# Kernel tuning notes

Hardware: AMD Instinct MI355X
Metric: run time of the kernel (lower is better)

## Reference

```python
import jax, jax.numpy as jnp
import numpy as np

B, T_ENC, T_DEC = 32, 128, 32
V_SRC, V_TGT = 32000, 32000
E_SRC, E_TGT = 256, 256
H_ENC, H_DEC, A = 512, 512, 8
CTX = 2 * H_ENC  # bidirectional encoder output dim


def setup_inputs():
    key = jax.random.key(0)
    ks = jax.random.split(key, 24)
    s = jnp.float32(0.02)

    def rn(k, shape):
        return jax.random.normal(k, shape, jnp.float32) * s

    return {
        'encoder_inputs': jax.random.randint(ks[0], (B, T_ENC), 0, V_SRC),
        'encoder_seq_length': jax.random.randint(ks[1], (B,), 1, T_ENC + 1),
        'decoder_inputs': jax.random.randint(ks[2], (B, T_DEC), 0, V_TGT),
        'decoder_seq_length': jax.random.randint(ks[3], (B,), 1, T_DEC + 1),
        'emb_src': rn(ks[4], (V_SRC, E_SRC)).at[0].set(0.0),  # padding_idx=0
        'emb_tgt': rn(ks[5], (V_TGT, E_TGT)).at[0].set(0.0),
        'Wih_f': rn(ks[6], (4 * H_ENC, E_SRC)), 'Whh_f': rn(ks[7], (4 * H_ENC, H_ENC)),
        'bih_f': rn(ks[8], (4 * H_ENC,)), 'bhh_f': rn(ks[9], (4 * H_ENC,)),
        'Wih_b': rn(ks[10], (4 * H_ENC, E_SRC)), 'Whh_b': rn(ks[11], (4 * H_ENC, H_ENC)),
        'bih_b': rn(ks[12], (4 * H_ENC,)), 'bhh_b': rn(ks[13], (4 * H_ENC,)),
        'gru_Wih': rn(ks[14], (3 * H_DEC, E_TGT + CTX)), 'gru_Whh': rn(ks[15], (3 * H_DEC, H_DEC)),
        'gru_bih': rn(ks[16], (3 * H_DEC,)), 'gru_bhh': rn(ks[17], (3 * H_DEC,)),
        'attn_W': rn(ks[18], (CTX + H_DEC, A)), 'attn_b': rn(ks[19], (A,)),
        'attn_v': rn(ks[20], (A,)),
        'clf_W': rn(ks[21], (V_TGT, H_DEC)), 'clf_b': rn(ks[22], (V_TGT,)),
    }


def _lstm(x_tbe, Wih, Whh, bih, bhh):
    # x_tbe: [T, B, E] -> hidden outputs [T, B, H]; PyTorch gate order i,f,g,o
    Bz = x_tbe.shape[1]
    h0 = jnp.zeros((Bz, H_ENC), x_tbe.dtype)

    def step(carry, xt):
        h, c = carry
        g = xt @ Wih.T + bih + h @ Whh.T + bhh
        i, f, gg, o = jnp.split(g, 4, axis=-1)
        c = jax.nn.sigmoid(f) * c + jax.nn.sigmoid(i) * jnp.tanh(gg)
        h = jax.nn.sigmoid(o) * jnp.tanh(c)
        return (h, c), h

    _, hs = jax.lax.scan(step, (h0, h0), x_tbe)
    return hs


def _gru(x, h, Wih, Whh, bih, bhh):
    # PyTorch GRUCell: gates r, z, n
    gi = x @ Wih.T + bih
    gh = h @ Whh.T + bhh
    ir, iz, inn = jnp.split(gi, 3, axis=-1)
    hr, hz, hn = jnp.split(gh, 3, axis=-1)
    r = jax.nn.sigmoid(ir + hr)
    z = jax.nn.sigmoid(iz + hz)
    n = jnp.tanh(inn + r * hn)
    return (1.0 - z) * n + z * h


def reference(encoder_inputs, encoder_seq_length, decoder_inputs, decoder_seq_length,
              emb_src, emb_tgt,
              Wih_f, Whh_f, bih_f, bhh_f, Wih_b, Whh_b, bih_b, bhh_b,
              gru_Wih, gru_Whh, gru_bih, gru_bhh,
              attn_W, attn_b, attn_v, clf_W, clf_b):
    lens = encoder_seq_length
    x = emb_src[encoder_inputs]                                   # [B,T,E]
    t = jnp.arange(T_ENC)[None, :]
    valid = t < lens[:, None]                                     # [B,T]

    # forward LSTM (padded steps masked out below; they never affect valid outputs)
    h_f = jnp.swapaxes(_lstm(jnp.swapaxes(x, 0, 1), Wih_f, Whh_f, bih_f, bhh_f), 0, 1)
    # backward LSTM: reverse each sequence within its true length
    rev = jnp.where(valid, lens[:, None] - 1 - t, t)              # [B,T]
    x_r = jnp.take_along_axis(x, rev[:, :, None], axis=1)
    h_b = jnp.swapaxes(_lstm(jnp.swapaxes(x_r, 0, 1), Wih_b, Whh_b, bih_b, bhh_b), 0, 1)
    h_b = jnp.take_along_axis(h_b, rev[:, :, None], axis=1)
    # pad_packed_sequence zeroes outputs past seq length
    enc_out = jnp.concatenate([h_f, h_b], axis=-1) * valid[:, :, None].astype(x.dtype)  # [B,T,2H]

    NEG = jnp.float32(-1e9)

    def step(h, tok):
        # ConcatAttention: v^T tanh(W [enc_out; state] + b), masked softmax
        feat = jnp.concatenate(
            [enc_out, jnp.broadcast_to(h[:, None, :], (B, T_ENC, H_DEC))], axis=-1)
        e = jnp.tanh(feat @ attn_W + attn_b) @ attn_v             # [B,T]
        a = jax.nn.softmax(jnp.where(valid, e, NEG), axis=-1)
        ctx = jnp.einsum('bt,btd->bd', a, enc_out)                # [B,2H]
        # pre-concat decoder: GRUCell([emb; ctx], h)
        xin = jnp.concatenate([emb_tgt[tok], ctx], axis=-1)
        h_new = _gru(xin, h, gru_Wih, gru_Whh, gru_bih, gru_bhh)
        logit = jax.nn.relu(h_new @ clf_W.T + clf_b)              # [B,V]
        return h_new, logit

    h0 = jnp.zeros((B, H_DEC), jnp.float32)
    _, outs = jax.lax.scan(step, h0, jnp.swapaxes(decoder_inputs, 0, 1))
    return jnp.swapaxes(outs, 0, 1)                               # [B,T_dec,V_tgt]
```

## Files before the change

kernel.cpp:

```cpp
#include <hip/hip_runtime.h>
#include <cmath>

#define NB   32
#define TE   128
#define TD   32
#define VOC  32000
#define EMB  256
#define HH   512
#define CTXD 1024
#define NR   1536

#define OHS  2048
#define OEO  (OHS + 2*129*NB*HH)
#define OEP  (OEO + NB*TE*CTXD)
#define OHD  (OEP + NB*TE*8)
#define OVEO (OHD + (TD+1)*NB*HH)
#define WSEND (OVEO + NB*NR*TE/2)

__device__ __forceinline__ float sigf(float x) { return 1.0f / (1.0f + expf(-x)); }
__device__ __forceinline__ float hsum4(float4 v) { return (v.x + v.y) + (v.z + v.w); }

__device__ __forceinline__ void stg1(float* p, float v) {
  __hip_atomic_store(p, v, __ATOMIC_RELAXED, __HIP_MEMORY_SCOPE_AGENT);
}

__device__ __forceinline__ void fma4(float4& a, const float4 w, const float4 u) {
  a.x = fmaf(w.x, u.x, a.x); a.y = fmaf(w.y, u.y, a.y);
  a.z = fmaf(w.z, u.z, a.z); a.w = fmaf(w.w, u.w, a.w);
}

__device__ __forceinline__ unsigned short to_bf16(float f) {
  unsigned int u = __float_as_uint(f);
  u = (u + 0x7FFF + ((u >> 16) & 1)) >> 16;
  return (unsigned short)u;
}

__device__ __forceinline__ void gbarG(int* bar, int idx, int target) {
  __syncthreads();
  if (threadIdx.x == 0) {
    __hip_atomic_fetch_add(bar + (idx & 7) * 16, 1,
                           __ATOMIC_RELAXED, __HIP_MEMORY_SCOPE_AGENT);
  }
  if (threadIdx.x < 64) {
    const int ln = threadIdx.x;
    int it = 0;
    while (true) {
      int v = (ln < 8)
        ? __hip_atomic_load(bar + ln * 16, __ATOMIC_RELAXED, __HIP_MEMORY_SCOPE_AGENT)
        : 0;
      v += __shfl_xor(v, 1); v += __shfl_xor(v, 2); v += __shfl_xor(v, 4);
      v = __shfl(v, 0);
      if (v >= target) break;
      __builtin_amdgcn_s_sleep(1);
      if (++it > (1 << 20)) break;
    }
  }
  __syncthreads();
}

__global__ void __launch_bounds__(512)
scan_kernel(const int* __restrict__ enc_in, const int* __restrict__ lens,
            const float* __restrict__ emb_src,
            const float* __restrict__ Wih_f, const float* __restrict__ Whh_f,
            const float* __restrict__ bih_f, const float* __restrict__ bhh_f,
            const float* __restrict__ Wih_b, const float* __restrict__ Whh_b,
            const float* __restrict__ bih_b, const float* __restrict__ bhh_b,
            float* __restrict__ ws)
{
  const int tid = threadIdx.x, bid = blockIdx.x;
  const int g = bid & 7, cg = bid >> 3;
  const int dir = g >> 2, bg = g & 3;
  int* bar = (int*)ws + g * 128;
  float* harr = ws + OHS;
  float* eo   = ws + OEO;

  asm volatile("buffer_inv sc1" ::: "memory");

  __shared__ int   tokL[TE][8];
  __shared__ float lds_p[8][4][68];

  for (int i = tid; i < TE * 8; i += 512) {
    int bb = i & 7, s = i >> 3;
    int b = bg * 8 + bb;
    int t = s;
    if (dir) { int L = lens[b]; t = (s < L) ? (L - 1 - s) : s; }
    tokL[s][bb] = enc_in[b * TE + t];
  }
  if (tid < 128) {
    int bb = tid >> 4, col = tid & 15;
    stg1(&harr[((size_t)(dir * 129) * NB + bg * 8 + bb) * HH + cg * 16 + col], 0.0f);
  }

  const int lane = tid & 63, w = tid >> 6;
  const int ks = w & 3, rh = w >> 2;
  const int rq = lane >> 4, kl = lane & 15;
  const int j0 = cg * 16;
  const float* Wih = dir ? Wih_b : Wih_f;
  const float* Whh = dir ? Whh_b : Whh_f;

  float4 Wreg[8][3];
  #pragma unroll
  for (int ri = 0; ri < 8; ++ri) {
    int r = rh * 32 + rq * 8 + ri;
    int o = (r >> 4) * HH + j0 + (r & 15);
    #pragma unroll
    for (int p = 0; p < 3; ++p) {
      int kf = (ks * 3 + p) * 16 + kl;
      Wreg[ri][p] = (kf < 64)
        ? *((const float4*)Wih + (size_t)o * 64 + kf)
        : *((const float4*)Whh + (size_t)o * 128 + (kf - 64));
    }
  }

  const int b_u = tid >> 4, col_u = tid & 15;
  const int j_u = j0 + col_u;
  const int bglob = bg * 8 + b_u;
  const int Lu = (tid < 128) ? lens[bglob] : 0;
  float bs0 = 0, bs1 = 0, bs2 = 0, bs3 = 0;
  if (tid < 128) {
    const float* bih = dir ? bih_b : bih_f;
    const float* bhh = dir ? bhh_b : bhh_f;
    bs0 = bih[j_u] + bhh[j_u];
    bs1 = bih[HH + j_u] + bhh[HH + j_u];
    bs2 = bih[2 * HH + j_u] + bhh[2 * HH + j_u];
    bs3 = bih[3 * HH + j_u] + bhh[3 * HH + j_u];
  }
  float cst = 0.0f;

  int tgt = 32;
  gbarG(bar, cg, tgt); tgt += 32;

  for (int s = 0; s < TE; ++s) {
    const float4* h4 = (const float4*)(harr + ((size_t)(dir * 129 + s) * NB) * HH);
    #pragma unroll 2
    for (int bb = 0; bb < 8; ++bb) {
      const int b = bg * 8 + bb;
      const int tok = tokL[s][bb];
      const float4* x4 = (const float4*)emb_src + (size_t)tok * 64;
      float4 u[3];
      #pragma unroll
      for (int p = 0; p < 3; ++p) {
        int c = ks * 3 + p;
        u[p] = (c < 4) ? x4[c * 16 + kl]
                       : h4[(size_t)b * 128 + (c - 4) * 16 + kl];
      }
      float sc[8];
      #pragma unroll
      for (int ri = 0; ri < 8; ++ri) {
        float4 a = {0, 0, 0, 0};
        fma4(a, Wreg[ri][0], u[0]);
        fma4(a, Wreg[ri][1], u[1]);
        fma4(a, Wreg[ri][2], u[2]);
        sc[ri] = hsum4(a);
      }
      #pragma unroll
      for (int ri = 0; ri < 8; ++ri) {
        sc[ri] += __shfl_xor(sc[ri], 1);
        sc[ri] += __shfl_xor(sc[ri], 2);
        sc[ri] += __shfl_xor(sc[ri], 4);
        sc[ri] += __shfl_xor(sc[ri], 8);
      }
      if (kl == 0) {
        int r0 = rh * 32 + rq * 8;
        float4 lo = {sc[0], sc[1], sc[2], sc[3]};
        float4 hi = {sc[4], sc[5], sc[6], sc[7]};
        *(float4*)&lds_p[bb][ks][r0]     = lo;
        *(float4*)&lds_p[bb][ks][r0 + 4] = hi;
      }
    }
    __syncthreads();

    if (tid < 128) {
      float gi = bs0, gf = bs1, gg = bs2, go = bs3;
      #pragma unroll
      for (int k2 = 0; k2 < 4; ++k2) {
        gi += lds_p[b_u][k2][col_u];
        gf += lds_p[b_u][k2][16 + col_u];
        gg += lds_p[b_u][k2][32 + col_u];
        go += lds_p[b_u][k2][48 + col_u];
      }
      float c = sigf(gf) * cst + sigf(gi) * tanhf(gg);
      cst = c;
      float h = sigf(go) * tanhf(c);
      stg1(&harr[((size_t)(dir * 129 + s + 1) * NB + bglob) * HH + j_u], h);
      float hm = (s < Lu) ? h : 0.0f;
      int pos = dir ? ((s < Lu) ? (Lu - 1 - s) : s) : s;
      eo[((size_t)bglob * TE + pos) * CTXD + dir * HH + j_u] = hm;
    }
    gbarG(bar, cg, tgt); tgt += 32;
  }
}

__global__ void __launch_bounds__(256)
veo_kernel(const float* __restrict__ eo, const float* __restrict__ gWih,
           unsigned short* __restrict__ veo)
{
  asm volatile("buffer_inv sc1" ::: "memory");
  __shared__ __align__(16) float As[16][132];
  __shared__ __align__(16) float Bs[16][132];
  const int tid = threadIdx.x;
  const int tx = tid & 15, ty = tid >> 4;
  const int n0 = blockIdx.x * 128, m0 = blockIdx.y * 128;
  float acc[8][8] = {};
  const int lr = tid >> 1;
  const int lk = (tid & 1) * 8;
  const float* arow = eo + (size_t)(m0 + lr) * CTXD;
  const float* brow = gWih + (size_t)(n0 + lr) * (EMB + CTXD) + EMB;

  for (int kc = 0; kc < CTXD; kc += 16) {
    float4 av0 = *(const float4*)&arow[kc + lk];
    float4 av1 = *(const float4*)&arow[kc + lk + 4];
    float4 bv0 = *(const float4*)&brow[kc + lk];
    float4 bv1 = *(const float4*)&brow[kc + lk + 4];
    __syncthreads();
    As[lk + 0][lr] = av0.x; As[lk + 1][lr] = av0.y;
    As[lk + 2][lr] = av0.z; As[lk + 3][lr] = av0.w;
    As[lk + 4][lr] = av1.x; As[lk + 5][lr] = av1.y;
    As[lk + 6][lr] = av1.z; As[lk + 7][lr] = av1.w;
    Bs[lk + 0][lr] = bv0.x; Bs[lk + 1][lr] = bv0.y;
    Bs[lk + 2][lr] = bv0.z; Bs[lk + 3][lr] = bv0.w;
    Bs[lk + 4][lr] = bv1.x; Bs[lk + 5][lr] = bv1.y;
    Bs[lk + 6][lr] = bv1.z; Bs[lk + 7][lr] = bv1.w;
    __syncthreads();
    #pragma unroll
    for (int kk = 0; kk < 16; ++kk) {
      float a8[8], b8[8];
      *(float4*)&a8[0] = *(const float4*)&As[kk][ty * 8];
      *(float4*)&a8[4] = *(const float4*)&As[kk][ty * 8 + 4];
      *(float4*)&b8[0] = *(const float4*)&Bs[kk][tx * 8];
      *(float4*)&b8[4] = *(const float4*)&Bs[kk][tx * 8 + 4];
      #pragma unroll
      for (int i = 0; i < 8; ++i)
        #pragma unroll
        for (int j = 0; j < 8; ++j)
          acc[i][j] = fmaf(a8[i], b8[j], acc[i][j]);
    }
  }
  const int b = m0 >> 7;
  #pragma unroll
  for (int j = 0; j < 8; ++j) {
    int n = n0 + tx * 8 + j;
    unsigned short o8[8];
    #pragma unroll
    for (int i = 0; i < 8; ++i) o8[i] = to_bf16(acc[i][j]);
    *(uint4*)&veo[((size_t)b * NR + n) * TE + ty * 8] = *(uint4*)o8;
  }
}

__global__ void __launch_bounds__(512)
dec_kernel(const int* __restrict__ dec_in, const int* __restrict__ lens,
           const float* __restrict__ emb_tgt,
           const float* __restrict__ gWih, const float* __restrict__ gWhh,
           const float* __restrict__ gbih, const float* __restrict__ gbhh,
           const float* __restrict__ attn_W, const float* __restrict__ attn_b,
           const float* __restrict__ attn_v,
           float* __restrict__ ws)
{
  const int tid = threadIdx.x, bid = blockIdx.x;
  const int g = bid & 7, cg = bid >> 3;
  const int B4 = g * 4;
  int* bar = (int*)ws + 1024 + g * 128;
  float* eo = ws + OEO;
  float* ep = ws + OEP;
  float* hd = ws + OHD;
  const unsigned short* veoH = (const unsigned short*)(ws + OVEO);

  asm volatile("buffer_inv sc1" ::: "memory");

  __shared__ float hl[4][520];
  __shared__ int   tokD[TD][4];
  __shared__ int   lensh[4];
  __shared__ float av8v[8];
  __shared__ float hpv[4][8];
  __shared__ float elds[4][128];
  __shared__ float wlds[4][128];
  __shared__ float mxs[4], invs[4];
  __shared__ float gvc[4][48];
  __shared__ float lds_pd[2][4][4][52];

  for (int i = tid; i < TD * 4; i += 512)
    tokD[i >> 2][i & 3] = dec_in[(B4 + (i & 3)) * TD + (i >> 2)];
  if (tid < 8) av8v[tid] = attn_v[tid];
  if (tid < 4) lensh[tid] = lens[B4 + tid];

  if (tid < 64) {
    int bb = tid >> 4, col = tid & 15;
    stg1(&hd[(size_t)(B4 + bb) * HH + cg * 16 + col], 0.0f);
  }

  {
    const int idx = cg * 512 + tid;
    if (idx < 4 * TE * 8) {
      int a = idx & 7, t = (idx >> 3) & 127, bb = idx >> 10;
      int b = B4 + bb;
      float acc = attn_b[a];
      const float* er = &eo[((size_t)b * TE + t) * CTXD];
      for (int d = 0; d < CTXD; d += 4) {
        float4 ev = *(const float4*)&er[d];
        acc = fmaf(ev.x, attn_W[(d + 0) * 8 + a], acc);
        acc = fmaf(ev.y, attn_W[(d + 1) * 8 + a], acc);
        acc = fmaf(ev.z, attn_W[(d + 2) * 8 + a], acc);
        acc = fmaf(ev.w, attn_W[(d + 3) * 8 + a], acc);
      }
      stg1(&ep[((size_t)b * TE + t) * 8 + a], acc);
    }
  }

  const int lane = tid & 63, w = tid >> 6;
  const int ks = w & 3, rh = w >> 2;
  const int rq = lane >> 4, kl = lane & 15;
  float4 Wreg[6][3];
  #pragma unroll
  for (int ri = 0; ri < 6; ++ri) {
    int rr = rh * 24 + rq * 6 + ri;
    int row = (rr >> 4) * HH + cg * 16 + (rr & 15);
    #pragma unroll
    for (int p = 0; p < 3; ++p) {
      int c = ks * 3 + p;
      Wreg[ri][p] = (c < 4)
        ? *(const float4*)(gWih + (size_t)row * (EMB + CTXD) + c * 64 + kl * 4)
        : *(const float4*)(gWhh + (size_t)row * HH + (c - 4) * 64 + kl * 4);
    }
  }

  const int ub = tid >> 4, ucol = tid & 15;
  const int uj = cg * 16 + ucol;
  float bRc = 0, bZc = 0, bNi = 0, bNh = 0;
  if (tid < 64) {
    bRc = gbih[uj] + gbhh[uj];
    bZc = gbih[HH + uj] + gbhh[HH + uj];
    bNi = gbih[2 * HH + uj];
    bNh = gbhh[2 * HH + uj];
  }

  int tgt = 32;
  gbarG(bar, cg, tgt); tgt += 32;

  for (int s = 0; s < TD; ++s) {
    {
      int bb = tid >> 7, c4 = (tid & 127) * 4;
      *(float4*)&hl[bb][c4] =
        *(const float4*)&hd[((size_t)s * NB + B4 + bb) * HH + c4];
    }
    __syncthreads();
    {
      const int bb = w >> 1;
      const float4* h4 = (const float4*)&hl[bb][0];
      float4 ha = h4[lane * 2], hb = h4[lane * 2 + 1];
      #pragma unroll
      for (int i = 0; i < 4; ++i) {
        const int a = (w & 1) * 4 + i;
        const float* wa = attn_W + (size_t)(CTXD + lane * 8) * 8 + a;
        float acc = 0.0f;
        acc = fmaf(ha.x, wa[0],  acc); acc = fmaf(ha.y, wa[8],  acc);
        acc = fmaf(ha.z, wa[16], acc); acc = fmaf(ha.w, wa[24], acc);
        acc = fmaf(hb.x, wa[32], acc); acc = fmaf(hb.y, wa[40], acc);
        acc = fmaf(hb.z, wa[48], acc); acc = fmaf(hb.w, wa[56], acc);
        acc += __shfl_xor(acc, 1);  acc += __shfl_xor(acc, 2);
        acc += __shfl_xor(acc, 4);  acc += __shfl_xor(acc, 8);
        acc += __shfl_xor(acc, 16); acc += __shfl_xor(acc, 32);
        if (lane == 0) hpv[bb][a] = acc;
      }
    }
    __syncthreads();
    {
      const int bb = tid >> 7, t = tid & 127;
      const int b = B4 + bb;
      float evv = -1e9f;
      if (t < lensh[bb]) {
        const float* e8 = &ep[((size_t)b * TE + t) * 8];
        float4 ea = *(const float4*)e8, eb2 = *(const float4*)(e8 + 4);
        evv  = tanhf(ea.x + hpv[bb][0]) * av8v[0];
        evv += tanhf(ea.y + hpv[bb][1]) * av8v[1];
        evv += tanhf(ea.z + hpv[bb][2]) * av8v[2];
        evv += tanhf(ea.w + hpv[bb][3]) * av8v[3];
        evv += tanhf(eb2.x + hpv[bb][4]) * av8v[4];
        evv += tanhf(eb2.y + hpv[bb][5]) * av8v[5];
        evv += tanhf(eb2.z + hpv[bb][6]) * av8v[6];
        evv += tanhf(eb2.w + hpv[bb][7]) * av8v[7];
      }
      elds[bb][t] = evv;
    }
    __syncthreads();
    if (tid < 256) {
      const int bb = tid >> 6, i = tid & 63;
      float m = fmaxf(elds[bb][i], elds[bb][i + 64]);
      m = fmaxf(m, __shfl_xor(m, 1));  m = fmaxf(m, __shfl_xor(m, 2));
      m = fmaxf(m, __shfl_xor(m, 4));  m = fmaxf(m, __shfl_xor(m, 8));
      m = fmaxf(m, __shfl_xor(m, 16)); m = fmaxf(m, __shfl_xor(m, 32));
      if (i == 0) mxs[bb] = m;
    }
    __syncthreads();
    {
      const int bb = tid >> 7, t = tid & 127;
      wlds[bb][t] = expf(elds[bb][t] - mxs[bb]);
    }
    __syncthreads();
    if (tid < 256) {
      const int bb = tid >> 6, i = tid & 63;
      float sm = wlds[bb][i] + wlds[bb][i + 64];
      sm += __shfl_xor(sm, 1);  sm += __shfl_xor(sm, 2);
      sm += __shfl_xor(sm, 4);  sm += __shfl_xor(sm, 8);
      sm += __shfl_xor(sm, 16); sm += __shfl_xor(sm, 32);
      if (i == 0) invs[bb] = 1.0f / sm;
    }
    {
      #pragma unroll
      for (int bb = 0; bb < 4; ++bb) {
        const float4* xr = (const float4*)(emb_tgt + (size_t)tokD[s][bb] * EMB);
        float4 u[3];
        #pragma unroll
        for (int p = 0; p < 3; ++p) {
          int c = ks * 3 + p;
          u[p] = (c < 4) ? xr[c * 16 + kl]
                         : *(const float4*)&hl[bb][(c - 4) * 64 + kl * 4];
        }
        float sI[6], sH[6];
        #pragma unroll
        for (int ri = 0; ri < 6; ++ri) {
          float4 aI = {0,0,0,0}, aH = {0,0,0,0};
          #pragma unroll
          for (int p = 0; p < 3; ++p) {
            int c = ks * 3 + p;
            if (c < 4) fma4(aI, Wreg[ri][p], u[p]);
            else       fma4(aH, Wreg[ri][p], u[p]);
          }
          sI[ri] = hsum4(aI); sH[ri] = hsum4(aH);
        }
        #pragma unroll
        for (int ri = 0; ri < 6; ++ri) {
          sI[ri] += __shfl_xor(sI[ri], 1); sH[ri] += __shfl_xor(sH[ri], 1);
          sI[ri] += __shfl_xor(sI[ri], 2); sH[ri] += __shfl_xor(sH[ri], 2);
          sI[ri] += __shfl_xor(sI[ri], 4); sH[ri] += __shfl_xor(sH[ri], 4);
          sI[ri] += __shfl_xor(sI[ri], 8); sH[ri] += __shfl_xor(sH[ri], 8);
        }
        if (kl == 0) {
          int r0 = rh * 24 + rq * 6;
          #pragma unroll
          for (int ri = 0; ri < 6; ++ri) {
            lds_pd[0][bb][ks][r0 + ri] = sI[ri];
            lds_pd[1][bb][ks][r0 + ri] = sH[ri];
          }
        }
      }
    }
    __syncthreads();
    if (tid < 384) {
      const int bb = tid / 96, idx = tid % 96;
      const int rr = idx >> 1, th = idx & 1;
      const int n = (rr >> 4) * HH + cg * 16 + (rr & 15);
      const unsigned short* vp = veoH + ((size_t)(B4 + bb) * NR + n) * TE + th * 64;
      const float* wl = &wlds[bb][th * 64];
      float acc = 0.0f;
      #pragma unroll
      for (int q = 0; q < 8; ++q) {
        uint4 pk = *(const uint4*)&vp[q * 8];
        unsigned int uu[4] = {pk.x, pk.y, pk.z, pk.w};
        #pragma unroll
        for (int h2 = 0; h2 < 4; ++h2) {
          acc = fmaf(wl[q * 8 + h2 * 2 + 0],
                     __uint_as_float((uu[h2] & 0xFFFFu) << 16), acc);
          acc = fmaf(wl[q * 8 + h2 * 2 + 1],
                     __uint_as_float((uu[h2] >> 16) << 16), acc);
        }
      }
      acc += __shfl_xor(acc, 1);
      if (th == 0) gvc[bb][rr] = acc * invs[bb];
    }
    __syncthreads();
    if (tid < 64) {
      float giR = gvc[ub][ucol], ghR = 0;
      float giZ = gvc[ub][16 + ucol], ghZ = 0;
      float giN = gvc[ub][32 + ucol], ghN = 0;
      #pragma unroll
      for (int k2 = 0; k2 < 4; ++k2) {
        giR += lds_pd[0][ub][k2][ucol];      ghR += lds_pd[1][ub][k2][ucol];
        giZ += lds_pd[0][ub][k2][16 + ucol]; ghZ += lds_pd[1][ub][k2][16 + ucol];
        giN += lds_pd[0][ub][k2][32 + ucol]; ghN += lds_pd[1][ub][k2][32 + ucol];
      }
      float r = sigf(giR + ghR + bRc);
      float z = sigf(giZ + ghZ + bZc);
      float n = tanhf(giN + bNi + r * (ghN + bNh));
      float hnew = (1.0f - z) * n + z * hl[ub][uj];
      stg1(&hd[((size_t)(s + 1) * NB + B4 + ub) * HH + uj], hnew);
    }
    gbarG(bar, cg, tgt); tgt += 32;
  }
}

__global__ void __launch_bounds__(256)
clf_kernel(const float* __restrict__ hd, const float* __restrict__ W,
           const float* __restrict__ bias, float* __restrict__ out)
{
  asm volatile("buffer_inv sc1" ::: "memory");
  __shared__ __align__(16) float As[16][132];
  __shared__ __align__(16) float Bs[16][132];
  const int tid = threadIdx.x;
  const int tx = tid & 15, ty = tid >> 4;
  const int n0 = blockIdx.x * 128, m0 = blockIdx.y * 128;
  float acc[8][8] = {};
  const int lr = tid >> 1;
  const int lk = (tid & 1) * 8;
  const int r  = m0 + lr;
  const float* arow = hd + ((size_t)((r & 31) + 1) * NB + (r >> 5)) * HH;
  const float* brow = W + (size_t)(n0 + lr) * HH;

  for (int kc = 0; kc < HH; kc += 16) {
    float4 av0 = *(const float4*)&arow[kc + lk];
    float4 av1 = *(const float4*)&arow[kc + lk + 4];
    float4 bv0 = *(const float4*)&brow[kc + lk];
    float4 bv1 = *(const float4*)&brow[kc + lk + 4];
    __syncthreads();
    As[lk + 0][lr] = av0.x; As[lk + 1][lr] = av0.y;
    As[lk + 2][lr] = av0.z; As[lk + 3][lr] = av0.w;
    As[lk + 4][lr] = av1.x; As[lk + 5][lr] = av1.y;
    As[lk + 6][lr] = av1.z; As[lk + 7][lr] = av1.w;
    Bs[lk + 0][lr] = bv0.x; Bs[lk + 1][lr] = bv0.y;
    Bs[lk + 2][lr] = bv0.z; Bs[lk + 3][lr] = bv0.w;
    Bs[lk + 4][lr] = bv1.x; Bs[lk + 5][lr] = bv1.y;
    Bs[lk + 6][lr] = bv1.z; Bs[lk + 7][lr] = bv1.w;
    __syncthreads();
    #pragma unroll
    for (int kk = 0; kk < 16; ++kk) {
      float a8[8], b8[8];
      *(float4*)&a8[0] = *(const float4*)&As[kk][ty * 8];
      *(float4*)&a8[4] = *(const float4*)&As[kk][ty * 8 + 4];
      *(float4*)&b8[0] = *(const float4*)&Bs[kk][tx * 8];
      *(float4*)&b8[4] = *(const float4*)&Bs[kk][tx * 8 + 4];
      #pragma unroll
      for (int i = 0; i < 8; ++i)
        #pragma unroll
        for (int j = 0; j < 8; ++j)
          acc[i][j] = fmaf(a8[i], b8[j], acc[i][j]);
    }
  }
  const int col = n0 + tx * 8;
  float bb[8];
  *(float4*)&bb[0] = *(const float4*)&bias[col];
  *(float4*)&bb[4] = *(const float4*)&bias[col + 4];
  #pragma unroll
  for (int i = 0; i < 8; ++i) {
    int row = m0 + ty * 8 + i;
    float4 o0, o1;
    o0.x = fmaxf(acc[i][0] + bb[0], 0.0f); o0.y = fmaxf(acc[i][1] + bb[1], 0.0f);
    o0.z = fmaxf(acc[i][2] + bb[2], 0.0f); o0.w = fmaxf(acc[i][3] + bb[3], 0.0f);
    o1.x = fmaxf(acc[i][4] + bb[4], 0.0f); o1.y = fmaxf(acc[i][5] + bb[5], 0.0f);
    o1.z = fmaxf(acc[i][6] + bb[6], 0.0f); o1.w = fmaxf(acc[i][7] + bb[7], 0.0f);
    *(float4*)&out[(size_t)row * VOC + col]     = o0;
    *(float4*)&out[(size_t)row * VOC + col + 4] = o1;
  }
}

extern "C" void kernel_launch(void* const* d_in, const int* in_sizes, int n_in,
                              void* d_out, int out_size, void* d_ws, size_t ws_size,
                              hipStream_t stream)
{
  if (ws_size < (size_t)WSEND * 4) return;

  const int* enc_in  = (const int*)d_in[0];
  const int* enc_len = (const int*)d_in[1];
  const int* dec_in  = (const int*)d_in[2];
  const float* emb_src = (const float*)d_in[4];
  const float* emb_tgt = (const float*)d_in[5];
  const float* Wih_f = (const float*)d_in[6];
  const float* Whh_f = (const float*)d_in[7];
  const float* bih_f = (const float*)d_in[8];
  const float* bhh_f = (const float*)d_in[9];
  const float* Wih_b = (const float*)d_in[10];
  const float* Whh_b = (const float*)d_in[11];
  const float* bih_b = (const float*)d_in[12];
  const float* bhh_b = (const float*)d_in[13];
  const float* gWih  = (const float*)d_in[14];
  const float* gWhh  = (const float*)d_in[15];
  const float* gbih  = (const float*)d_in[16];
  const float* gbhh  = (const float*)d_in[17];
  const float* attn_W = (const float*)d_in[18];
  const float* attn_b = (const float*)d_in[19];
  const float* attn_v = (const float*)d_in[20];
  const float* clf_W = (const float*)d_in[21];
  const float* clf_b = (const float*)d_in[22];
  float* ws  = (float*)d_ws;
  float* out = (float*)d_out;

  hipMemsetAsync(d_ws, 0, 8192, stream);
  scan_kernel<<<256, 512, 0, stream>>>(enc_in, enc_len, emb_src,
      Wih_f, Whh_f, bih_f, bhh_f, Wih_b, Whh_b, bih_b, bhh_b, ws);
  veo_kernel<<<dim3(NR / 128, (NB * TE) / 128), 256, 0, stream>>>(
      ws + OEO, gWih, (unsigned short*)(ws + OVEO));
  dec_kernel<<<256, 512, 0, stream>>>(dec_in, enc_len, emb_tgt,
      gWih, gWhh, gbih, gbhh, attn_W, attn_b, attn_v, ws);
  dim3 cg(VOC / 128, (NB * TD) / 128);
  clf_kernel<<<cg, 256, 0, stream>>>(ws + OHD, clf_W, clf_b, out);
}
```

Baseline: 2.334 ms.

## Overlap encoder input projection with grid barrier; classifier GEMM via split-bf16 MFMA

The encoder LSTM scan splits the grid barrier into arrive and wait phases. The next step's input-embedding projection is computed into LDS between them, so only the recurrent h·Whh part stays on the critical path after the barrier. Separately, the classifier GEMM is rewritten from FP32 FMA tiling to bf16 MFMA 16x16x32, using a hi/lo split (three MFMAs per tile) to keep near-fp32 accuracy. This adds conversion overhead and drops LDS staging, so each wave reads global memory directly.

```diff
diff --git a/kernel.cpp b/kernel.cpp
--- a/kernel.cpp
+++ b/kernel.cpp
@@ -17,6 +17,9 @@
 #define OVEO (OHD + (TD+1)*NB*HH)
 #define WSEND (OVEO + NB*NR*TE/2)
 
+typedef __attribute__((ext_vector_type(8))) short bf16x8;
+typedef __attribute__((ext_vector_type(4))) float f32x4;
+
 __device__ __forceinline__ float sigf(float x) { return 1.0f / (1.0f + expf(-x)); }
 __device__ __forceinline__ float hsum4(float4 v) { return (v.x + v.y) + (v.z + v.w); }
 
@@ -33,6 +36,12 @@
   unsigned int u = __float_as_uint(f);
   u = (u + 0x7FFF + ((u >> 16) & 1)) >> 16;
   return (unsigned short)u;
+}
+__device__ __forceinline__ void cvt_split(float x, short& hi, short& lo) {
+  unsigned short h = to_bf16(x);
+  float fh = __uint_as_float(((unsigned int)h) << 16);
+  hi = (short)h;
+  lo = (short)to_bf16(x - fh);
 }
 
 __device__ __forceinline__ void gbarG(int* bar, int idx, int target) {
@@ -41,6 +50,30 @@
     __hip_atomic_fetch_add(bar + (idx & 7) * 16, 1,
                            __ATOMIC_RELAXED, __HIP_MEMORY_SCOPE_AGENT);
   }
+  if (threadIdx.x < 64) {
+    const int ln = threadIdx.x;
+    int it = 0;
+    while (true) {
+      int v = (ln < 8)
+        ? __hip_atomic_load(bar + ln * 16, __ATOMIC_RELAXED, __HIP_MEMORY_SCOPE_AGENT)
+        : 0;
+      v += __shfl_xor(v, 1); v += __shfl_xor(v, 2); v += __shfl_xor(v, 4);
+      v = __shfl(v, 0);
+      if (v >= target) break;
+      __builtin_amdgcn_s_sleep(1);
+      if (++it > (1 << 20)) break;
+    }
+  }
+  __syncthreads();
+}
+__device__ __forceinline__ void gbarArrive(int* bar, int idx) {
+  __syncthreads();
+  if (threadIdx.x == 0) {
+    __hip_atomic_fetch_add(bar + (idx & 7) * 16, 1,
+                           __ATOMIC_RELAXED, __HIP_MEMORY_SCOPE_AGENT);
+  }
+}
+__device__ __forceinline__ void gbarWaitS(int* bar, int target) {
   if (threadIdx.x < 64) {
     const int ln = threadIdx.x;
     int it = 0;
@@ -103,13 +136,9 @@
   for (int ri = 0; ri < 8; ++ri) {
     int r = rh * 32 + rq * 8 + ri;
     int o = (r >> 4) * HH + j0 + (r & 15);
-    #pragma unroll
-    for (int p = 0; p < 3; ++p) {
-      int kf = (ks * 3 + p) * 16 + kl;
-      Wreg[ri][p] = (kf < 64)
-        ? *((const float4*)Wih + (size_t)o * 64 + kf)
-        : *((const float4*)Whh + (size_t)o * 128 + (kf - 64));
-    }
+    Wreg[ri][0] = *((const float4*)Wih + (size_t)o * 64 + ks * 16 + kl);
+    Wreg[ri][1] = *((const float4*)Whh + (size_t)o * 128 + (2 * ks) * 16 + kl);
+    Wreg[ri][2] = *((const float4*)Whh + (size_t)o * 128 + (2 * ks + 1) * 16 + kl);
   }
 
   const int b_u = tid >> 4, col_u = tid & 15;
@@ -127,45 +156,72 @@
   }
   float cst = 0.0f;
 
-  int tgt = 32;
-  gbarG(bar, cg, tgt); tgt += 32;
-
-  for (int s = 0; s < TE; ++s) {
-    const float4* h4 = (const float4*)(harr + ((size_t)(dir * 129 + s) * NB) * HH);
+  auto SHADOW = [&](int s) {
     #pragma unroll 2
     for (int bb = 0; bb < 8; ++bb) {
-      const int b = bg * 8 + bb;
       const int tok = tokL[s][bb];
-      const float4* x4 = (const float4*)emb_src + (size_t)tok * 64;
-      float4 u[3];
-      #pragma unroll
-      for (int p = 0; p < 3; ++p) {
-        int c = ks * 3 + p;
-        u[p] = (c < 4) ? x4[c * 16 + kl]
-                       : h4[(size_t)b * 128 + (c - 4) * 16 + kl];
-      }
-      float sc[8];
+      float4 ux = *((const float4*)emb_src + (size_t)tok * 64 + ks * 16 + kl);
+      float sx[8];
       #pragma unroll
       for (int ri = 0; ri < 8; ++ri) {
         float4 a = {0, 0, 0, 0};
-        fma4(a, Wreg[ri][0], u[0]);
-        fma4(a, Wreg[ri][1], u[1]);
-        fma4(a, Wreg[ri][2], u[2]);
-        sc[ri] = hsum4(a);
+        fma4(a, Wreg[ri][0], ux);
+        sx[ri] = hsum4(a);
       }
       #pragma unroll
       for (int ri = 0; ri < 8; ++ri) {
-        sc[ri] += __shfl_xor(sc[ri], 1);
-        sc[ri] += __shfl_xor(sc[ri], 2);
-        sc[ri] += __shfl_xor(sc[ri], 4);
-        sc[ri] += __shfl_xor(sc[ri], 8);
+        sx[ri] += __shfl_xor(sx[ri], 1);
+        sx[ri] += __shfl_xor(sx[ri], 2);
+        sx[ri] += __shfl_xor(sx[ri], 4);
+        sx[ri] += __shfl_xor(sx[ri], 8);
       }
       if (kl == 0) {
         int r0 = rh * 32 + rq * 8;
-        float4 lo = {sc[0], sc[1], sc[2], sc[3]};
-        float4 hi = {sc[4], sc[5], sc[6], sc[7]};
+        float4 lo = {sx[0], sx[1], sx[2], sx[3]};
+        float4 hi = {sx[4], sx[5], sx[6], sx[7]};
         *(float4*)&lds_p[bb][ks][r0]     = lo;
         *(float4*)&lds_p[bb][ks][r0 + 4] = hi;
+      }
+    }
+  };
+
+  gbarArrive(bar, cg);
+  SHADOW(0);
+  gbarWaitS(bar, 32);
+  int tgt = 64;
+
+  for (int s = 0; s < TE; ++s) {
+    {
+      const float4* h4 = (const float4*)(harr + ((size_t)(dir * 129 + s) * NB) * HH);
+      #pragma unroll 2
+      for (int bb = 0; bb < 8; ++bb) {
+        const int b = bg * 8 + bb;
+        float4 u0 = h4[(size_t)b * 128 + (2 * ks) * 16 + kl];
+        float4 u1 = h4[(size_t)b * 128 + (2 * ks + 1) * 16 + kl];
+        float sc[8];
+        #pragma unroll
+        for (int ri = 0; ri < 8; ++ri) {
+          float4 a = {0, 0, 0, 0};
+          fma4(a, Wreg[ri][1], u0);
+          fma4(a, Wreg[ri][2], u1);
+          sc[ri] = hsum4(a);
+        }
+        #pragma unroll
+        for (int ri = 0; ri < 8; ++ri) {
+          sc[ri] += __shfl_xor(sc[ri], 1);
+          sc[ri] += __shfl_xor(sc[ri], 2);
+          sc[ri] += __shfl_xor(sc[ri], 4);
+          sc[ri] += __shfl_xor(sc[ri], 8);
+        }
+        if (kl == 0) {
+          int r0 = rh * 32 + rq * 8;
+          float4 lo = *(float4*)&lds_p[bb][ks][r0];
+          float4 hi = *(float4*)&lds_p[bb][ks][r0 + 4];
+          lo.x += sc[0]; lo.y += sc[1]; lo.z += sc[2]; lo.w += sc[3];
+          hi.x += sc[4]; hi.y += sc[5]; hi.z += sc[6]; hi.w += sc[7];
+          *(float4*)&lds_p[bb][ks][r0]     = lo;
+          *(float4*)&lds_p[bb][ks][r0 + 4] = hi;
+        }
       }
     }
     __syncthreads();
@@ -187,7 +243,9 @@
       int pos = dir ? ((s < Lu) ? (Lu - 1 - s) : s) : s;
       eo[((size_t)bglob * TE + pos) * CTXD + dir * HH + j_u] = hm;
     }
-    gbarG(bar, cg, tgt); tgt += 32;
+    gbarArrive(bar, cg);
+    if (s + 1 < TE) SHADOW(s + 1);
+    gbarWaitS(bar, tgt); tgt += 32;
   }
 }
 
@@ -493,61 +551,50 @@
            const float* __restrict__ bias, float* __restrict__ out)
 {
   asm volatile("buffer_inv sc1" ::: "memory");
-  __shared__ __align__(16) float As[16][132];
-  __shared__ __align__(16) float Bs[16][132];
   const int tid = threadIdx.x;
-  const int tx = tid & 15, ty = tid >> 4;
-  const int n0 = blockIdx.x * 128, m0 = blockIdx.y * 128;
-  float acc[8][8] = {};
-  const int lr = tid >> 1;
-  const int lk = (tid & 1) * 8;
-  const int r  = m0 + lr;
-  const float* arow = hd + ((size_t)((r & 31) + 1) * NB + (r >> 5)) * HH;
-  const float* brow = W + (size_t)(n0 + lr) * HH;
-
-  for (int kc = 0; kc < HH; kc += 16) {
-    float4 av0 = *(const float4*)&arow[kc + lk];
-    float4 av1 = *(const float4*)&arow[kc + lk + 4];
-    float4 bv0 = *(const float4*)&brow[kc + lk];
-    float4 bv1 = *(const float4*)&brow[kc + lk + 4];
-    __syncthreads();
-    As[lk + 0][lr] = av0.x; As[lk + 1][lr] = av0.y;
-    As[lk + 2][lr] = av0.z; As[lk + 3][lr] = av0.w;
-    As[lk + 4][lr] = av1.x; As[lk + 5][lr] = av1.y;
-    As[lk + 6][lr] = av1.z; As[lk + 7][lr] = av1.w;
-    Bs[lk + 0][lr] = bv0.x; Bs[lk + 1][lr] = bv0.y;
-    Bs[lk + 2][lr] = bv0.z; Bs[lk + 3][lr] = bv0.w;
-    Bs[lk + 4][lr] = bv1.x; Bs[lk + 5][lr] = bv1.y;
-    Bs[lk + 6][lr] = bv1.z; Bs[lk + 7][lr] = bv1.w;
-    __syncthreads();
+  const int wv = tid >> 6, l = tid & 63;
+  const int lr = l & 15, lk = (l >> 4) * 8;
+  const int n0 = blockIdx.x * 64 + wv * 16;
+  const int m0 = blockIdx.y * 64;
+  const float* arow[4];
+  #pragma unroll
+  for (int ms = 0; ms < 4; ++ms) {
+    int r = m0 + ms * 16 + lr;
+    arow[ms] = hd + ((size_t)((r & 31) + 1) * NB + (r >> 5)) * HH + lk;
+  }
+  const float* brow = W + (size_t)(n0 + lr) * HH + lk;
+  f32x4 acc[4] = {};
+
+  for (int kc = 0; kc < HH; kc += 32) {
+    bf16x8 bh, bl;
+    {
+      float4 b0 = *(const float4*)&brow[kc];
+      float4 b1 = *(const float4*)&brow[kc + 4];
+      float bf[8] = {b0.x, b0.y, b0.z, b0.w, b1.x, b1.y, b1.z, b1.w};
+      #pragma unroll
+      for (int i = 0; i < 8; ++i) { short h, lo2; cvt_split(bf[i], h, lo2); bh[i] = h; bl[i] = lo2; }
+    }
     #pragma unroll
-    for (int kk = 0; kk < 16; ++kk) {
-      float a8[8], b8[8];
-      *(float4*)&a8[0] = *(const float4*)&As[kk][ty * 8];
-      *(float4*)&a8[4] = *(const float4*)&As[kk][ty * 8 + 4];
-      *(float4*)&b8[0] = *(const float4*)&Bs[kk][tx * 8];
-      *(float4*)&b8[4] = *(const float4*)&Bs[kk][tx * 8 + 4];
-      #pragma unroll
-      for (int i = 0; i < 8; ++i)
-        #pragma unroll
-        for (int j = 0; j < 8; ++j)
-          acc[i][j] = fmaf(a8[i], b8[j], acc[i][j]);
-    }
-  }
-  const int col = n0 + tx * 8;
-  float bb[8];
-  *(float4*)&bb[0] = *(const float4*)&bias[col];
-  *(float4*)&bb[4] = *(const float4*)&bias[col + 4];
+    for (int ms = 0; ms < 4; ++ms) {
+      float4 a0 = *(const float4*)&arow[ms][kc];
+      float4 a1 = *(const float4*)&arow[ms][kc + 4];
+      float af[8] = {a0.x, a0.y, a0.z, a0.w, a1.x, a1.y, a1.z, a1.w};
+      bf16x8 ah, al;
+      #pragma unroll
+      for (int i = 0; i < 8; ++i) { short h, lo2; cvt_split(af[i], h, lo2); ah[i] = h; al[i] = lo2; }
+      acc[ms] = __builtin_amdgcn_mfma_f32_16x16x32_bf16(ah, bh, acc[ms], 0, 0, 0);
+      acc[ms] = __builtin_amdgcn_mfma_f32_16x16x32_bf16(ah, bl, acc[ms], 0, 0, 0);
+      acc[ms] = __builtin_amdgcn_mfma_f32_16x16x32_bf16(al, bh, acc[ms], 0, 0, 0);
+    }
+  }
+  const float bn = bias[n0 + lr];
   #pragma unroll
-  for (int i = 0; i < 8; ++i) {
-    int row = m0 + ty * 8 + i;
-    float4 o0, o1;
-    o0.x = fmaxf(acc[i][0] + bb[0], 0.0f); o0.y = fmaxf(acc[i][1] + bb[1], 0.0f);
-    o0.z = fmaxf(acc[i][2] + bb[2], 0.0f); o0.w = fmaxf(acc[i][3] + bb[3], 0.0f);
-    o1.x = fmaxf(acc[i][4] + bb[4], 0.0f); o1.y = fmaxf(acc[i][5] + bb[5], 0.0f);
-    o1.z = fmaxf(acc[i][6] + bb[6], 0.0f); o1.w = fmaxf(acc[i][7] + bb[7], 0.0f);
-    *(float4*)&out[(size_t)row * VOC + col]     = o0;
-    *(float4*)&out[(size_t)row * VOC + col + 4] = o1;
+  for (int ms = 0; ms < 4; ++ms) {
+    #pragma unroll
+    for (int r = 0; r < 4; ++r) {
+      int m = m0 + ms * 16 + (l >> 4) * 4 + r;
+      out[(size_t)m * VOC + n0 + lr] = fmaxf(acc[ms][r] + bn, 0.0f);
+    }
   }
 }
 
@@ -589,6 +636,6 @@
       ws + OEO, gWih, (unsigned short*)(ws + OVEO));
   dec_kernel<<<256, 512, 0, stream>>>(dec_in, enc_len, emb_tgt,
       gWih, gWhh, gbih, gbhh, attn_W, attn_b, attn_v, ws);
-  dim3 cg(VOC / 128, (NB * TD) / 128);
+  dim3 cg(VOC / 64, (NB * TD) / 64);
   clf_kernel<<<cg, 256, 0, stream>>>(ws + OHD, clf_W, clf_b, out);
 }
```

After: 3.166 ms. +35.7%, slower.

## Run classifier GEMM on bf16 MFMA with split-bf16 activations

Applied to the files above, without the earlier changes.

Replaces the fp32 SIMT classifier GEMM with a bf16 MFMA kernel. A new conversion kernel splits the decoder hidden states into high and low bf16 parts. The classifier converts weights to bf16 on the fly and accumulates two MFMAs per tile (hi and lo activations). M tiles grow to 256 rows so each weight tile is reused more. Weights are rounded to plain bf16 without a low-part correction, so accuracy drops versus fp32. The output stores are per-element and scattered rather than vectorized.

```diff
diff --git a/kernel.cpp b/kernel.cpp
--- a/kernel.cpp
+++ b/kernel.cpp
@@ -16,6 +16,9 @@
 #define OHD  (OEP + NB*TE*8)
 #define OVEO (OHD + (TD+1)*NB*HH)
 #define WSEND (OVEO + NB*NR*TE/2)
+
+typedef __attribute__((ext_vector_type(8))) short bf16x8;
+typedef __attribute__((ext_vector_type(4))) float f32x4;
 
 __device__ __forceinline__ float sigf(float x) { return 1.0f / (1.0f + expf(-x)); }
 __device__ __forceinline__ float hsum4(float4 v) { return (v.x + v.y) + (v.z + v.w); }
@@ -489,65 +492,96 @@
 }
 
 __global__ void __launch_bounds__(256)
-clf_kernel(const float* __restrict__ hd, const float* __restrict__ W,
-           const float* __restrict__ bias, float* __restrict__ out)
+conv_kernel(const float* __restrict__ hd,
+            unsigned short* __restrict__ Abh, unsigned short* __restrict__ Abl)
 {
   asm volatile("buffer_inv sc1" ::: "memory");
-  __shared__ __align__(16) float As[16][132];
-  __shared__ __align__(16) float Bs[16][132];
-  const int tid = threadIdx.x;
-  const int tx = tid & 15, ty = tid >> 4;
-  const int n0 = blockIdx.x * 128, m0 = blockIdx.y * 128;
-  float acc[8][8] = {};
-  const int lr = tid >> 1;
-  const int lk = (tid & 1) * 8;
-  const int r  = m0 + lr;
-  const float* arow = hd + ((size_t)((r & 31) + 1) * NB + (r >> 5)) * HH;
-  const float* brow = W + (size_t)(n0 + lr) * HH;
-
-  for (int kc = 0; kc < HH; kc += 16) {
-    float4 av0 = *(const float4*)&arow[kc + lk];
-    float4 av1 = *(const float4*)&arow[kc + lk + 4];
-    float4 bv0 = *(const float4*)&brow[kc + lk];
-    float4 bv1 = *(const float4*)&brow[kc + lk + 4];
-    __syncthreads();
-    As[lk + 0][lr] = av0.x; As[lk + 1][lr] = av0.y;
-    As[lk + 2][lr] = av0.z; As[lk + 3][lr] = av0.w;
-    As[lk + 4][lr] = av1.x; As[lk + 5][lr] = av1.y;
-    As[lk + 6][lr] = av1.z; As[lk + 7][lr] = av1.w;
-    Bs[lk + 0][lr] = bv0.x; Bs[lk + 1][lr] = bv0.y;
-    Bs[lk + 2][lr] = bv0.z; Bs[lk + 3][lr] = bv0.w;
-    Bs[lk + 4][lr] = bv1.x; Bs[lk + 5][lr] = bv1.y;
-    Bs[lk + 6][lr] = bv1.z; Bs[lk + 7][lr] = bv1.w;
-    __syncthreads();
-    #pragma unroll
-    for (int kk = 0; kk < 16; ++kk) {
-      float a8[8], b8[8];
-      *(float4*)&a8[0] = *(const float4*)&As[kk][ty * 8];
-      *(float4*)&a8[4] = *(const float4*)&As[kk][ty * 8 + 4];
-      *(float4*)&b8[0] = *(const float4*)&Bs[kk][tx * 8];
-      *(float4*)&b8[4] = *(const float4*)&Bs[kk][tx * 8 + 4];
-      #pragma unroll
-      for (int i = 0; i < 8; ++i)
-        #pragma unroll
-        for (int j = 0; j < 8; ++j)
-          acc[i][j] = fmaf(a8[i], b8[j], acc[i][j]);
-    }
-  }
-  const int col = n0 + tx * 8;
-  float bb[8];
-  *(float4*)&bb[0] = *(const float4*)&bias[col];
-  *(float4*)&bb[4] = *(const float4*)&bias[col + 4];
+  const int idx = blockIdx.x * 256 + threadIdx.x;
+  const int m = idx >> 6;
+  const int k8 = (idx & 63) * 8;
+  const float* src = hd + ((size_t)((m & 31) + 1) * NB + (m >> 5)) * HH + k8;
+  float4 a0 = *(const float4*)src;
+  float4 a1 = *(const float4*)(src + 4);
+  float f[8] = {a0.x, a0.y, a0.z, a0.w, a1.x, a1.y, a1.z, a1.w};
+  unsigned short hi[8], lo[8];
   #pragma unroll
   for (int i = 0; i < 8; ++i) {
-    int row = m0 + ty * 8 + i;
-    float4 o0, o1;
-    o0.x = fmaxf(acc[i][0] + bb[0], 0.0f); o0.y = fmaxf(acc[i][1] + bb[1], 0.0f);
-    o0.z = fmaxf(acc[i][2] + bb[2], 0.0f); o0.w = fmaxf(acc[i][3] + bb[3], 0.0f);
-    o1.x = fmaxf(acc[i][4] + bb[4], 0.0f); o1.y = fmaxf(acc[i][5] + bb[5], 0.0f);
-    o1.z = fmaxf(acc[i][6] + bb[6], 0.0f); o1.w = fmaxf(acc[i][7] + bb[7], 0.0f);
-    *(float4*)&out[(size_t)row * VOC + col]     = o0;
-    *(float4*)&out[(size_t)row * VOC + col + 4] = o1;
+    unsigned short h = to_bf16(f[i]);
+    float fh = __uint_as_float(((unsigned int)h) << 16);
+    hi[i] = h;
+    lo[i] = to_bf16(f[i] - fh);
+  }
+  *(uint4*)&Abh[(size_t)m * HH + k8] = *(uint4*)hi;
+  *(uint4*)&Abl[(size_t)m * HH + k8] = *(uint4*)lo;
+}
+
+__global__ void __launch_bounds__(256)
+clf_kernel(const unsigned short* __restrict__ Abh, const unsigned short* __restrict__ Abl,
+           const float* __restrict__ W, const float* __restrict__ bias,
+           float* __restrict__ out)
+{
+  asm volatile("buffer_inv sc1" ::: "memory");
+  __shared__ __align__(16) unsigned short Ah[256][40];
+  __shared__ __align__(16) unsigned short Al[256][40];
+  __shared__ __align__(16) unsigned short Wh[128][40];
+  const int tid = threadIdx.x;
+  const int wv = tid >> 6, l = tid & 63;
+  const int lr = l & 15, lkq = l >> 4;
+  const int n0 = blockIdx.x * 128, m0 = blockIdx.y * 256;
+  f32x4 acc[2][16] = {};
+
+  for (int kc = 0; kc < HH; kc += 32) {
+    __syncthreads();
+    {
+      const unsigned short* sh = Abh + (size_t)(m0 + tid) * HH + kc;
+      const unsigned short* sl = Abl + (size_t)(m0 + tid) * HH + kc;
+      uint4 h0 = *(const uint4*)(sh);      uint4 h1 = *(const uint4*)(sh + 8);
+      uint4 h2 = *(const uint4*)(sh + 16); uint4 h3 = *(const uint4*)(sh + 24);
+      uint4 l0 = *(const uint4*)(sl);      uint4 l1 = *(const uint4*)(sl + 8);
+      uint4 l2 = *(const uint4*)(sl + 16); uint4 l3 = *(const uint4*)(sl + 24);
+      *(uint4*)&Ah[tid][0]  = h0; *(uint4*)&Ah[tid][8]  = h1;
+      *(uint4*)&Ah[tid][16] = h2; *(uint4*)&Ah[tid][24] = h3;
+      *(uint4*)&Al[tid][0]  = l0; *(uint4*)&Al[tid][8]  = l1;
+      *(uint4*)&Al[tid][16] = l2; *(uint4*)&Al[tid][24] = l3;
+      const int wr = tid >> 1, hf = tid & 1;
+      const float* wsrc = W + (size_t)(n0 + wr) * HH + kc + hf * 16;
+      unsigned int o[8];
+      #pragma unroll
+      for (int i = 0; i < 16; i += 4) {
+        float4 v = *(const float4*)&wsrc[i];
+        o[(i >> 1) + 0] = (unsigned int)to_bf16(v.x) | ((unsigned int)to_bf16(v.y) << 16);
+        o[(i >> 1) + 1] = (unsigned int)to_bf16(v.z) | ((unsigned int)to_bf16(v.w) << 16);
+      }
+      *(uint4*)&Wh[wr][hf * 16]     = *(uint4*)&o[0];
+      *(uint4*)&Wh[wr][hf * 16 + 8] = *(uint4*)&o[4];
+    }
+    __syncthreads();
+    bf16x8 bfr[2];
+    bfr[0] = *(const bf16x8*)&Wh[wv * 32 + lr][lkq * 8];
+    bfr[1] = *(const bf16x8*)&Wh[wv * 32 + 16 + lr][lkq * 8];
+    #pragma unroll
+    for (int mf = 0; mf < 16; ++mf) {
+      bf16x8 ah = *(const bf16x8*)&Ah[mf * 16 + lr][lkq * 8];
+      bf16x8 al = *(const bf16x8*)&Al[mf * 16 + lr][lkq * 8];
+      #pragma unroll
+      for (int nf = 0; nf < 2; ++nf) {
+        acc[nf][mf] = __builtin_amdgcn_mfma_f32_16x16x32_bf16(ah, bfr[nf], acc[nf][mf], 0, 0, 0);
+        acc[nf][mf] = __builtin_amdgcn_mfma_f32_16x16x32_bf16(al, bfr[nf], acc[nf][mf], 0, 0, 0);
+      }
+    }
+  }
+  #pragma unroll
+  for (int nf = 0; nf < 2; ++nf) {
+    const int n = n0 + wv * 32 + nf * 16 + lr;
+    const float bn = bias[n];
+    #pragma unroll
+    for (int mf = 0; mf < 16; ++mf) {
+      #pragma unroll
+      for (int r = 0; r < 4; ++r) {
+        int m = m0 + mf * 16 + lkq * 4 + r;
+        out[(size_t)m * VOC + n] = fmaxf(acc[nf][mf][r] + bn, 0.0f);
+      }
+    }
   }
 }
 
@@ -582,6 +616,9 @@
   float* ws  = (float*)d_ws;
   float* out = (float*)d_out;
 
+  unsigned short* Abh = (unsigned short*)(ws + OHS);
+  unsigned short* Abl = Abh + (size_t)NB * TD * HH;
+
   hipMemsetAsync(d_ws, 0, 8192, stream);
   scan_kernel<<<256, 512, 0, stream>>>(enc_in, enc_len, emb_src,
       Wih_f, Whh_f, bih_f, bhh_f, Wih_b, Whh_b, bih_b, bhh_b, ws);
@@ -589,6 +626,7 @@
       ws + OEO, gWih, (unsigned short*)(ws + OVEO));
   dec_kernel<<<256, 512, 0, stream>>>(dec_in, enc_len, emb_tgt,
       gWih, gWhh, gbih, gbhh, attn_W, attn_b, attn_v, ws);
-  dim3 cg(VOC / 128, (NB * TD) / 128);
-  clf_kernel<<<cg, 256, 0, stream>>>(ws + OHD, clf_W, clf_b, out);
-}
+  conv_kernel<<<256, 256, 0, stream>>>(ws + OHD, Abh, Abl);
+  dim3 cg(VOC / 128, (NB * TD) / 256);
+  clf_kernel<<<cg, 256, 0, stream>>>(Abh, Abl, clf_W, clf_b, out);
+}
```

Result: faster. 2.157 ms (-7.6%).
